# Kernel optimization log

Hardware: AMD Instinct MI355X
Metric: run time of the kernel (lower is better)

Reference implementation:

```python
import jax, jax.numpy as jnp
import numpy as np

DECAY = 0.99


def setup_inputs() -> dict:
    key = jax.random.key(0)
    k1, k2, k3 = jax.random.split(key, 3)
    B, L, D, N = 8, 2048, 512, 1024
    x = jax.random.normal(k1, (B, L, D), dtype=jnp.float32)
    codebook = jax.random.normal(k2, (N, D), dtype=jnp.float32)
    ema_weight = jax.random.normal(k3, (N, D), dtype=jnp.float32)
    counts = jnp.ones((N,), dtype=jnp.float32)
    return {"x": x, "codebook": codebook, "ema_weight": ema_weight, "counts": counts}


def reference(x, codebook, ema_weight, counts):
    # x: [B, L, D]; codebook/ema_weight: [N, D]; counts: [N]
    n_tokens = codebook.shape[0]
    # avoids materializing the [B,L,N,D] difference tensor of the naive form)
    x_sq = jnp.sum(x * x, axis=-1, keepdims=True)            # [B, L, 1]
    c_sq = jnp.sum(codebook * codebook, axis=-1)             # [N]
    xc = jnp.einsum('bld,nd->bln', x, codebook)              # [B, L, N]
    distances = jnp.sqrt(jnp.maximum(x_sq - 2.0 * xc + c_sq, 0.0))
    indices = jnp.argmin(distances, axis=-1)                 # [B, L]
    encodings = jax.nn.one_hot(indices, n_tokens, dtype=jnp.float32)  # [B, L, N]
    # train=True branch: EMA codebook update
    counts_new = DECAY * counts + (1.0 - DECAY) * jnp.sum(encodings, axis=(0, 1))
    dw = jnp.einsum('bln,bld->nd', encodings, x)             # [N, D]
    ema_new = DECAY * ema_weight + (1.0 - DECAY) * dw
    codebook_new = ema_new / counts_new[:, None]
    # quantization with straight-through estimator
    quantized = jnp.einsum('bln,nd->bld', encodings, codebook_new)  # [B, L, D]
    quantized = x + jax.lax.stop_gradient(quantized - x)
    # optax.l2_loss(x, quantized) = 0.5 * (x - quantized)^2
    codebook_loss = jnp.mean(0.5 * jnp.square(x - quantized))
    return quantized, codebook_loss, indices
```

## Files before the change

kernel.cpp:

```cpp
#include <hip/hip_runtime.h>
#include <hip/hip_bf16.h>

constexpr int Dd   = 512;
constexpr int Nn   = 1024;
constexpr int Ttok = 16384;
constexpr float DECAYc = 0.99f;
constexpr float MARGIN = 10.0f;
constexpr int CH = 16;

typedef short bf16x8 __attribute__((ext_vector_type(8)));
typedef float f32x4  __attribute__((ext_vector_type(4)));
typedef unsigned short us8v __attribute__((ext_vector_type(8)));

__device__ inline unsigned short f2bf(float f) {
  unsigned int b = __float_as_uint(f);
  return (unsigned short)((b + 0x7FFFu + ((b >> 16) & 1u)) >> 16);
}
__device__ inline float bf2f(unsigned short u) {
  return __uint_as_float(((unsigned int)u) << 16);
}

__global__ __launch_bounds__(64) void k_prep_cb(const float* __restrict__ cb,
                                                unsigned short* __restrict__ cbh,
                                                float* __restrict__ csq) {
  const int n = blockIdx.x, l = threadIdx.x;
  const float4* r = (const float4*)(cb + (size_t)n * Dd);
  float4 a = r[l], b = r[l + 64];
  float ss = a.x*a.x + a.y*a.y + a.z*a.z + a.w*a.w
           + b.x*b.x + b.y*b.y + b.z*b.z + b.w*b.w;
  ushort4 ua, ub;
  ua.x = f2bf(a.x); ua.y = f2bf(a.y); ua.z = f2bf(a.z); ua.w = f2bf(a.w);
  ub.x = f2bf(b.x); ub.y = f2bf(b.y); ub.z = f2bf(b.z); ub.w = f2bf(b.w);
  ((ushort4*)(cbh + (size_t)n * Dd))[l]      = ua;
  ((ushort4*)(cbh + (size_t)n * Dd))[l + 64] = ub;
#pragma unroll
  for (int o = 32; o; o >>= 1) ss += __shfl_down(ss, o);
  if (l == 0) csq[n] = ss;
}

__global__ __launch_bounds__(256) void k_gemm_scores(
    const unsigned short* __restrict__ cbh, const float* __restrict__ x,
    const float* __restrict__ csq, unsigned short* __restrict__ S) {
  __shared__ unsigned short As[128 * 64];
  __shared__ unsigned short Bs[128 * 64];
  const int tid = threadIdx.x;
  const int w = tid >> 6, l = tid & 63;
  const int b = blockIdx.x;
  const int s = (b & 7) * 128 + (b >> 3);
  const int cm = s & 7;
  const int tn = s >> 3;
  const int wr = w >> 1, wc = w & 1;

  const int srow = tid >> 3;
  const int xorw = (tid >> 3) & 7;
  const int scolA = ((tid & 7) ^ xorw) * 8;
  const int scolB = (tid & 7) * 8;
  const int wcolB = ((tid & 7) ^ xorw) * 8;

  f32x4 acc[4][4] = {};

  const unsigned short* gA0 = cbh + (size_t)(cm * 128) * Dd;
  const float*          gB0 = x   + (size_t)(tn * 128) * Dd;

  us8v bq[4];
#define LOADB(KC) do {                                                        \
    const int k0_ = (KC) * 64;                                                \
    _Pragma("unroll")                                                         \
    for (int p = 0; p < 4; ++p) {                                             \
      const float* gb = gB0 + (size_t)(p * 32 + srow) * Dd + k0_ + scolB;     \
      float4 v0 = *(const float4*)gb;                                         \
      float4 v1 = *(const float4*)(gb + 4);                                   \
      us8v o;                                                                 \
      o[0]=f2bf(v0.x); o[1]=f2bf(v0.y); o[2]=f2bf(v0.z); o[3]=f2bf(v0.w);     \
      o[4]=f2bf(v1.x); o[5]=f2bf(v1.y); o[6]=f2bf(v1.z); o[7]=f2bf(v1.w);     \
      bq[p] = o;                                                              \
    }                                                                         \
  } while (0)

  LOADB(0);

  for (int kc = 0; kc < Dd / 64; ++kc) {
    const int k0 = kc * 64;
    __syncthreads();
#pragma unroll
    for (int c = 0; c < 4; ++c) {
      const unsigned short* ga = gA0 + (size_t)(c * 32 + srow) * Dd + k0 + scolA;
      char* la = (char*)As + c * 4096 + w * 1024;
      __builtin_amdgcn_global_load_lds((const __attribute__((address_space(1))) void*)ga,
                                       (__attribute__((address_space(3))) void*)la, 16, 0, 0);
    }
#pragma unroll
    for (int p = 0; p < 4; ++p)
      *(us8v*)&Bs[(p * 32 + srow) * 64 + wcolB] = bq[p];
    __syncthreads();
    if (kc + 1 < Dd / 64) LOADB(kc + 1);
#pragma unroll
    for (int ks = 0; ks < 2; ++ks) {
      const int ra = l & 15;
      const int rx = l & 7;
      const int kbs = ((ks * 4 + (l >> 4)) ^ rx) * 8;
      bf16x8 af[4], bfr[4];
#pragma unroll
      for (int m = 0; m < 4; ++m)
        af[m] = *(const bf16x8*)&As[(wr * 64 + m * 16 + ra) * 64 + kbs];
#pragma unroll
      for (int n = 0; n < 4; ++n)
        bfr[n] = *(const bf16x8*)&Bs[(wc * 64 + n * 16 + ra) * 64 + kbs];
#pragma unroll
      for (int m = 0; m < 4; ++m)
#pragma unroll
        for (int n = 0; n < 4; ++n)
          acc[m][n] = __builtin_amdgcn_mfma_f32_16x16x32_bf16(af[m], bfr[n], acc[m][n], 0, 0, 0);
    }
  }
#undef LOADB

  const int code0 = cm * 128 + wr * 64 + (l >> 4) * 4;
  const int tok0  = tn * 128 + wc * 64 + (l & 15);
#pragma unroll
  for (int m = 0; m < 4; ++m) {
    const int cd = code0 + m * 16;
    float4 cs = *(const float4*)&csq[cd];
#pragma unroll
    for (int n = 0; n < 4; ++n) {
      const int tk = tok0 + n * 16;
      ushort4 o;
      o.x = f2bf(cs.x - 2.0f * acc[m][n][0]);
      o.y = f2bf(cs.y - 2.0f * acc[m][n][1]);
      o.z = f2bf(cs.z - 2.0f * acc[m][n][2]);
      o.w = f2bf(cs.w - 2.0f * acc[m][n][3]);
      *(ushort4*)(S + (size_t)tk * Nn + cd) = o;
    }
  }
}

__global__ __launch_bounds__(256) void k_scan(
    const unsigned short* __restrict__ S, const float* __restrict__ x,
    const float* __restrict__ cb, const float* __restrict__ csq,
    int* __restrict__ idxb, float* __restrict__ idxf, float* __restrict__ hist) {
  __shared__ int candn[4][32];
  __shared__ int ccnt[4];
  const int tid = threadIdx.x, wid = tid >> 6, l = tid & 63;
  const int t = blockIdx.x * 4 + wid;

  const unsigned short* row = S + (size_t)t * Nn;
  us8v c0 = *(const us8v*)(row + l * 8);
  us8v c1 = *(const us8v*)(row + 512 + l * 8);
  float f0[8], f1[8];
  float minv = 3.4e38f; int mini = 0;
#pragma unroll
  for (int j = 0; j < 8; ++j) {
    f0[j] = bf2f(c0[j]);
    if (f0[j] < minv) { minv = f0[j]; mini = l * 8 + j; }
  }
#pragma unroll
  for (int j = 0; j < 8; ++j) {
    f1[j] = bf2f(c1[j]);
    if (f1[j] < minv) { minv = f1[j]; mini = 512 + l * 8 + j; }
  }
#pragma unroll
  for (int o = 1; o < 64; o <<= 1) {
    float ov = __shfl_xor(minv, o); int oi = __shfl_xor(mini, o);
    if (ov < minv || (ov == minv && oi < mini)) { minv = ov; mini = oi; }
  }
  if (l == 0) ccnt[wid] = 0;
  const float thr = minv + MARGIN;
#pragma unroll
  for (int j = 0; j < 8; ++j)
    if (f0[j] <= thr) { int p = atomicAdd(&ccnt[wid], 1); if (p < 32) candn[wid][p] = l * 8 + j; }
#pragma unroll
  for (int j = 0; j < 8; ++j)
    if (f1[j] <= thr) { int p = atomicAdd(&ccnt[wid], 1); if (p < 32) candn[wid][p] = 512 + l * 8 + j; }
  int nc = ccnt[wid]; if (nc > 32) nc = 32;

  int besti;
  if (nc == 1) {
    besti = candn[wid][0];
  } else {
    float bestv = 3.4e38f; besti = 0x7fffffff;
    const float4* xr = (const float4*)(x + (size_t)t * Dd);
    float4 xa = xr[l * 2], xb = xr[l * 2 + 1];
    for (int c = 0; c < nc; ++c) {
      int n = candn[wid][c];
      const float4* cr = (const float4*)(cb + (size_t)n * Dd);
      float4 ca = cr[l * 2], cb4 = cr[l * 2 + 1];
      float p = xa.x*ca.x + xa.y*ca.y + xa.z*ca.z + xa.w*ca.w
              + xb.x*cb4.x + xb.y*cb4.y + xb.z*cb4.z + xb.w*cb4.w;
#pragma unroll
      for (int o = 32; o; o >>= 1) p += __shfl_xor(p, o);
      float sc = csq[n] - 2.0f * p;
      if (sc < bestv || (sc == bestv && n < besti)) { bestv = sc; besti = n; }
    }
  }
  if (l == 0) {
    idxb[t] = besti;
    idxf[t] = (float)besti;
    atomicAdd(&hist[besti], 1.0f);
  }
}

__global__ __launch_bounds__(256) void k_offsets(const float* __restrict__ hist,
                                                 int* __restrict__ offs,
                                                 int* __restrict__ cursor) {
  __shared__ int wsum[4];
  const int tid = threadIdx.x, l = tid & 63, wd = tid >> 6;
  const int base = tid * 4;
  int c0 = (int)hist[base], c1 = (int)hist[base + 1],
      c2 = (int)hist[base + 2], c3 = (int)hist[base + 3];
  int sum = c0 + c1 + c2 + c3;
  int sc = sum;
#pragma unroll
  for (int o = 1; o < 64; o <<= 1) { int v = __shfl_up(sc, o); if (l >= o) sc += v; }
  if (l == 63) wsum[wd] = sc;
  __syncthreads();
  int wbase = 0;
  for (int i = 0; i < wd; ++i) wbase += wsum[i];
  int e = wbase + sc - sum;
  offs[base] = e;     cursor[base] = e;
  offs[base+1] = e + c0; cursor[base+1] = e + c0;
  offs[base+2] = e + c0 + c1; cursor[base+2] = e + c0 + c1;
  offs[base+3] = e + c0 + c1 + c2; cursor[base+3] = e + c0 + c1 + c2;
}

__global__ __launch_bounds__(256) void k_scatter(const int* __restrict__ idxb,
                                                 int* __restrict__ cursor,
                                                 int* __restrict__ bucket,
                                                 int* __restrict__ bcode) {
  int t = blockIdx.x * 256 + threadIdx.x;
  if (t < Ttok) {
    int n = idxb[t];
    int p = atomicAdd(&cursor[n], 1);
    bucket[p] = t;
    bcode[p] = n;
  }
}

__global__ __launch_bounds__(512) void k_dw_part(
    const float* __restrict__ x, const int* __restrict__ bucket,
    const int* __restrict__ bcode, float* __restrict__ dw) {
  __shared__ int sh_t[CH], sh_n[CH];
  const int tid = threadIdx.x;
  const int p0 = blockIdx.x * CH;
  if (tid < CH) { sh_t[tid] = bucket[p0 + tid]; sh_n[tid] = bcode[p0 + tid]; }
  __syncthreads();
  float v[CH];
#pragma unroll
  for (int j = 0; j < CH; ++j)
    v[j] = x[(size_t)sh_t[j] * Dd + tid];
  float acc = v[0]; int cur = sh_n[0];
#pragma unroll
  for (int j = 1; j < CH; ++j) {
    int n = sh_n[j];
    if (n != cur) { atomicAdd(&dw[(size_t)cur * Dd + tid], acc); acc = 0.f; cur = n; }
    acc += v[j];
  }
  atomicAdd(&dw[(size_t)cur * Dd + tid], acc);
}

__global__ __launch_bounds__(256) void finalize_cb(
    const float* __restrict__ ema, const float* __restrict__ dw,
    const float* __restrict__ counts, const float* __restrict__ hist,
    float* __restrict__ cbnew) {
  int e4 = blockIdx.x * 256 + threadIdx.x;
  int n = e4 >> 7;
  float cnt = DECAYc * counts[n] + (1.0f - DECAYc) * hist[n];
  float inv = 1.0f / cnt;
  float4 e = ((const float4*)ema)[e4];
  float4 d = ((const float4*)dw)[e4];
  float4 o;
  o.x = (DECAYc * e.x + (1.0f - DECAYc) * d.x) * inv;
  o.y = (DECAYc * e.y + (1.0f - DECAYc) * d.y) * inv;
  o.z = (DECAYc * e.z + (1.0f - DECAYc) * d.z) * inv;
  o.w = (DECAYc * e.w + (1.0f - DECAYc) * d.w) * inv;
  ((float4*)cbnew)[e4] = o;
}

__global__ __launch_bounds__(256) void quant_loss(
    const float* __restrict__ x, const float* __restrict__ cbnew,
    const int* __restrict__ idx, float* __restrict__ out_q,
    float* __restrict__ loss) {
  const int e0 = blockIdx.x * 256 + threadIdx.x;
  const int gsz = 524288;
  int n[4]; float4 q[4], xv[4];
#pragma unroll
  for (int j = 0; j < 4; ++j) n[j] = idx[(e0 + j * gsz) >> 7];
#pragma unroll
  for (int j = 0; j < 4; ++j) {
    const int e = e0 + j * gsz;
    q[j]  = ((const float4*)(cbnew + (size_t)n[j] * Dd))[e & 127];
    xv[j] = ((const float4*)x)[e];
  }
  float part = 0.f;
#pragma unroll
  for (int j = 0; j < 4; ++j) {
    ((float4*)out_q)[e0 + j * gsz] = q[j];
    float dx = xv[j].x - q[j].x, dy = xv[j].y - q[j].y,
          dz = xv[j].z - q[j].z, dw_ = xv[j].w - q[j].w;
    part += dx*dx + dy*dy + dz*dz + dw_*dw_;
  }
  __shared__ float red[4];
#pragma unroll
  for (int o = 32; o; o >>= 1) part += __shfl_down(part, o);
  int wid = threadIdx.x >> 6, lane = threadIdx.x & 63;
  if (lane == 0) red[wid] = part;
  __syncthreads();
  if (threadIdx.x == 0) atomicAdd(loss, red[0] + red[1] + red[2] + red[3]);
}

__global__ void loss_final(const float* __restrict__ loss,
                           float* __restrict__ out_loss) {
  *out_loss = loss[0] * (0.5f / (float)((size_t)Ttok * Dd));
}

extern "C" void kernel_launch(void* const* d_in, const int* in_sizes, int n_in,
                              void* d_out, int out_size, void* d_ws, size_t ws_size,
                              hipStream_t stream) {
  const float* x      = (const float*)d_in[0];
  const float* cb     = (const float*)d_in[1];
  const float* ema    = (const float*)d_in[2];
  const float* counts = (const float*)d_in[3];

  float* out      = (float*)d_out;
  float* q_out    = out;
  float* loss_out = out + (size_t)Ttok * Dd;
  float* idxf_out = loss_out + 1;
  unsigned short* S = (unsigned short*)q_out;

  float* ws = (float*)d_ws;
  unsigned short* cbh = (unsigned short*)ws;
  float* dw      = ws + 262144;
  float* hist    = ws + 786432;
  float* loss    = ws + 787456;
  float* csq     = ws + 787460;
  int*   offs    = (int*)(ws + 788484);
  int*   cursor  = (int*)(ws + 789508);
  int*   bucket  = (int*)(ws + 790532);
  int*   bcode   = (int*)(ws + 806916);
  int*   idxb    = (int*)(ws + 823300);
  float* cbnew   = ws + 839684;

  hipMemsetAsync(dw, 0, (size_t)525316 * sizeof(float), stream);

  k_prep_cb<<<Nn, 64, 0, stream>>>(cb, cbh, csq);
  k_gemm_scores<<<(Nn / 128) * (Ttok / 128), 256, 0, stream>>>(cbh, x, csq, S);
  k_scan<<<Ttok / 4, 256, 0, stream>>>(S, x, cb, csq, idxb, idxf_out, hist);
  k_offsets<<<1, 256, 0, stream>>>(hist, offs, cursor);
  k_scatter<<<Ttok / 256, 256, 0, stream>>>(idxb, cursor, bucket, bcode);
  k_dw_part<<<Ttok / CH, 512, 0, stream>>>(x, bucket, bcode, dw);
  finalize_cb<<<(Nn * Dd / 4) / 256, 256, 0, stream>>>(ema, dw, counts, hist, cbnew);
  quant_loss<<<2048, 256, 0, stream>>>(x, cbnew, idxb, q_out, loss);
  loss_final<<<1, 1, 0, stream>>>(loss, loss_out);
}
```

Baseline: 126.5 us.

## Fuse top-2 argmin reduction into score GEMM epilogue and double-buffer A tiles

The GEMM epilogue no longer writes the full bf16 score matrix. For each 128-code slice it computes a per-token top-2 with a count of near-minimum candidates and writes one compact float4 per token. A new select kernel merges the 8 slices and rescores the few candidates exactly in fp32, falling back to a full 128-code rescan when a slice has many near-ties. This removes the large score-matrix write and read. It also double-buffers the codebook LDS tile so the next A load overlaps compute, at the cost of more shared memory and extra epilogue work.

Result: slower. 495.9 us (+291.9%).

```diff
diff --git a/kernel.cpp b/kernel.cpp
--- a/kernel.cpp
+++ b/kernel.cpp
@@ -15,9 +15,6 @@
 __device__ inline unsigned short f2bf(float f) {
   unsigned int b = __float_as_uint(f);
   return (unsigned short)((b + 0x7FFFu + ((b >> 16) & 1u)) >> 16);
-}
-__device__ inline float bf2f(unsigned short u) {
-  return __uint_as_float(((unsigned int)u) << 16);
 }
 
 __global__ __launch_bounds__(64) void k_prep_cb(const float* __restrict__ cb,
@@ -40,9 +37,10 @@
 
 __global__ __launch_bounds__(256) void k_gemm_scores(
     const unsigned short* __restrict__ cbh, const float* __restrict__ x,
-    const float* __restrict__ csq, unsigned short* __restrict__ S) {
-  __shared__ unsigned short As[128 * 64];
+    const float* __restrict__ csq, float4* __restrict__ part) {
+  __shared__ unsigned short As[2][128 * 64];
   __shared__ unsigned short Bs[128 * 64];
+  __shared__ float4 red4[2][128];
   const int tid = threadIdx.x;
   const int w = tid >> 6, l = tid & 63;
   const int b = blockIdx.x;
@@ -68,32 +66,39 @@
     _Pragma("unroll")                                                         \
     for (int p = 0; p < 4; ++p) {                                             \
       const float* gb = gB0 + (size_t)(p * 32 + srow) * Dd + k0_ + scolB;     \
-      float4 v0 = *(const float4*)gb;                                         \
-      float4 v1 = *(const float4*)(gb + 4);                                   \
+      float4 v0_ = *(const float4*)gb;                                        \
+      float4 v1_ = *(const float4*)(gb + 4);                                  \
       us8v o;                                                                 \
-      o[0]=f2bf(v0.x); o[1]=f2bf(v0.y); o[2]=f2bf(v0.z); o[3]=f2bf(v0.w);     \
-      o[4]=f2bf(v1.x); o[5]=f2bf(v1.y); o[6]=f2bf(v1.z); o[7]=f2bf(v1.w);     \
+      o[0]=f2bf(v0_.x); o[1]=f2bf(v0_.y); o[2]=f2bf(v0_.z); o[3]=f2bf(v0_.w); \
+      o[4]=f2bf(v1_.x); o[5]=f2bf(v1_.y); o[6]=f2bf(v1_.z); o[7]=f2bf(v1_.w); \
       bq[p] = o;                                                              \
     }                                                                         \
   } while (0)
-
+#define ISSUEA(KC, BUF) do {                                                  \
+    const int k0_ = (KC) * 64;                                                \
+    _Pragma("unroll")                                                         \
+    for (int c = 0; c < 4; ++c) {                                             \
+      const unsigned short* ga = gA0 + (size_t)(c * 32 + srow) * Dd + k0_ + scolA; \
+      char* la = (char*)&As[BUF][0] + c * 4096 + w * 1024;                    \
+      __builtin_amdgcn_global_load_lds((const __attribute__((address_space(1))) void*)ga, \
+                                       (__attribute__((address_space(3))) void*)la, 16, 0, 0); \
+    }                                                                         \
+  } while (0)
+
+  ISSUEA(0, 0);
   LOADB(0);
 
   for (int kc = 0; kc < Dd / 64; ++kc) {
-    const int k0 = kc * 64;
     __syncthreads();
-#pragma unroll
-    for (int c = 0; c < 4; ++c) {
-      const unsigned short* ga = gA0 + (size_t)(c * 32 + srow) * Dd + k0 + scolA;
-      char* la = (char*)As + c * 4096 + w * 1024;
-      __builtin_amdgcn_global_load_lds((const __attribute__((address_space(1))) void*)ga,
-                                       (__attribute__((address_space(3))) void*)la, 16, 0, 0);
-    }
 #pragma unroll
     for (int p = 0; p < 4; ++p)
       *(us8v*)&Bs[(p * 32 + srow) * 64 + wcolB] = bq[p];
     __syncthreads();
-    if (kc + 1 < Dd / 64) LOADB(kc + 1);
+    if (kc + 1 < Dd / 64) {
+      ISSUEA(kc + 1, (kc + 1) & 1);
+      LOADB(kc + 1);
+    }
+    const unsigned short* Ab = &As[kc & 1][0];
 #pragma unroll
     for (int ks = 0; ks < 2; ++ks) {
       const int ra = l & 15;
@@ -102,7 +107,7 @@
       bf16x8 af[4], bfr[4];
 #pragma unroll
       for (int m = 0; m < 4; ++m)
-        af[m] = *(const bf16x8*)&As[(wr * 64 + m * 16 + ra) * 64 + kbs];
+        af[m] = *(const bf16x8*)&Ab[(wr * 64 + m * 16 + ra) * 64 + kbs];
 #pragma unroll
       for (int n = 0; n < 4; ++n)
         bfr[n] = *(const bf16x8*)&Bs[(wc * 64 + n * 16 + ra) * 64 + kbs];
@@ -114,82 +119,116 @@
     }
   }
 #undef LOADB
-
-  const int code0 = cm * 128 + wr * 64 + (l >> 4) * 4;
-  const int tok0  = tn * 128 + wc * 64 + (l & 15);
-#pragma unroll
-  for (int m = 0; m < 4; ++m) {
-    const int cd = code0 + m * 16;
-    float4 cs = *(const float4*)&csq[cd];
-#pragma unroll
-    for (int n = 0; n < 4; ++n) {
-      const int tk = tok0 + n * 16;
-      ushort4 o;
-      o.x = f2bf(cs.x - 2.0f * acc[m][n][0]);
-      o.y = f2bf(cs.y - 2.0f * acc[m][n][1]);
-      o.z = f2bf(cs.z - 2.0f * acc[m][n][2]);
-      o.w = f2bf(cs.w - 2.0f * acc[m][n][3]);
-      *(ushort4*)(S + (size_t)tk * Nn + cd) = o;
-    }
-  }
-}
-
-__global__ __launch_bounds__(256) void k_scan(
-    const unsigned short* __restrict__ S, const float* __restrict__ x,
+#undef ISSUEA
+
+  const int base4 = wr * 64 + (l >> 4) * 4;
+  float4 cs[4];
+#pragma unroll
+  for (int m = 0; m < 4; ++m)
+    cs[m] = *(const float4*)&csq[cm * 128 + base4 + m * 16];
+
+#pragma unroll
+  for (int n = 0; n < 4; ++n) {
+    float v0 = 3.4e38f, v1 = 3.4e38f;
+    int i0 = 0x7fffffff, i1 = 0x7fffffff;
+#pragma unroll
+    for (int m = 0; m < 4; ++m) {
+#pragma unroll
+      for (int r = 0; r < 4; ++r) {
+        float sv = fmaf(-2.0f, acc[m][n][r], ((const float*)&cs[m])[r]);
+        int idx = cm * 128 + base4 + m * 16 + r;
+        if (sv < v0)      { v1 = v0; i1 = i0; v0 = sv; i0 = idx; }
+        else if (sv < v1) { v1 = sv; i1 = idx; }
+      }
+    }
+#pragma unroll
+    for (int o = 16; o <= 32; o <<= 1) {
+      float b0 = __shfl_xor(v0, o), b1 = __shfl_xor(v1, o);
+      int  bi0 = __shfl_xor(i0, o), bi1 = __shfl_xor(i1, o);
+      bool bf = (b0 < v0) || (b0 == v0 && bi0 < i0);
+      float lo = bf ? v0 : b0; int loi = bf ? i0 : bi0;
+      float w1 = bf ? b1 : v1; int w1i = bf ? bi1 : i1;
+      if (bf) { v0 = b0; i0 = bi0; }
+      bool sf = (lo < w1) || (lo == w1 && loi < w1i);
+      v1 = sf ? lo : w1; i1 = sf ? loi : w1i;
+    }
+    int c16 = 0; const float thr = v0 + MARGIN;
+#pragma unroll
+    for (int m = 0; m < 4; ++m)
+#pragma unroll
+      for (int r = 0; r < 4; ++r)
+        c16 += (fmaf(-2.0f, acc[m][n][r], ((const float*)&cs[m])[r]) <= thr) ? 1 : 0;
+    c16 += __shfl_xor(c16, 16); c16 += __shfl_xor(c16, 32);
+    if ((l >> 4) == 0)
+      red4[wr][wc * 64 + n * 16 + l] = make_float4(
+          v0, v1, __uint_as_float((unsigned)i0 | ((unsigned)i1 << 16)),
+          __uint_as_float((unsigned)c16));
+  }
+  __syncthreads();
+  if (tid < 128) {
+    float4 a = red4[0][tid], e = red4[1][tid];
+    unsigned au = __float_as_uint(a.z), eu = __float_as_uint(e.z);
+    int ai0 = au & 0xffff, ai1 = au >> 16;
+    int ei0 = eu & 0xffff, ei1 = eu >> 16;
+    bool bf = (e.x < a.x) || (e.x == a.x && ei0 < ai0);
+    float v0 = bf ? e.x : a.x; int i0 = bf ? ei0 : ai0;
+    float lo = bf ? a.x : e.x; int loi = bf ? ai0 : ei0;
+    float w1 = bf ? e.y : a.y; int w1i = bf ? ei1 : ai1;
+    bool sf = (lo < w1) || (lo == w1 && loi < w1i);
+    float v1 = sf ? lo : w1; int i1 = sf ? loi : w1i;
+    unsigned cnt = __float_as_uint(a.w) + __float_as_uint(e.w);
+    part[(size_t)cm * Ttok + tn * 128 + tid] = make_float4(
+        v0, v1, __uint_as_float((unsigned)i0 | ((unsigned)i1 << 16)),
+        __uint_as_float(cnt));
+  }
+}
+
+__device__ inline void rescore(int n, const float4& xa, const float4& xb,
+                               const float* __restrict__ cb,
+                               const float* __restrict__ csq, int l,
+                               float& bestv, int& besti) {
+  const float4* cr = (const float4*)(cb + (size_t)n * Dd);
+  float4 ca = cr[l * 2], cc = cr[l * 2 + 1];
+  float p = xa.x*ca.x + xa.y*ca.y + xa.z*ca.z + xa.w*ca.w
+          + xb.x*cc.x + xb.y*cc.y + xb.z*cc.z + xb.w*cc.w;
+#pragma unroll
+  for (int o = 32; o; o >>= 1) p += __shfl_xor(p, o);
+  float sc = csq[n] - 2.0f * p;
+  if (sc < bestv || (sc == bestv && n < besti)) { bestv = sc; besti = n; }
+}
+
+__global__ __launch_bounds__(256) void k_select(
+    const float4* __restrict__ part, const float* __restrict__ x,
     const float* __restrict__ cb, const float* __restrict__ csq,
     int* __restrict__ idxb, float* __restrict__ idxf, float* __restrict__ hist) {
-  __shared__ int candn[4][32];
-  __shared__ int ccnt[4];
   const int tid = threadIdx.x, wid = tid >> 6, l = tid & 63;
   const int t = blockIdx.x * 4 + wid;
-
-  const unsigned short* row = S + (size_t)t * Nn;
-  us8v c0 = *(const us8v*)(row + l * 8);
-  us8v c1 = *(const us8v*)(row + 512 + l * 8);
-  float f0[8], f1[8];
-  float minv = 3.4e38f; int mini = 0;
-#pragma unroll
-  for (int j = 0; j < 8; ++j) {
-    f0[j] = bf2f(c0[j]);
-    if (f0[j] < minv) { minv = f0[j]; mini = l * 8 + j; }
-  }
-#pragma unroll
-  for (int j = 0; j < 8; ++j) {
-    f1[j] = bf2f(c1[j]);
-    if (f1[j] < minv) { minv = f1[j]; mini = 512 + l * 8 + j; }
-  }
-#pragma unroll
-  for (int o = 1; o < 64; o <<= 1) {
-    float ov = __shfl_xor(minv, o); int oi = __shfl_xor(mini, o);
-    if (ov < minv || (ov == minv && oi < mini)) { minv = ov; mini = oi; }
-  }
-  if (l == 0) ccnt[wid] = 0;
-  const float thr = minv + MARGIN;
-#pragma unroll
-  for (int j = 0; j < 8; ++j)
-    if (f0[j] <= thr) { int p = atomicAdd(&ccnt[wid], 1); if (p < 32) candn[wid][p] = l * 8 + j; }
-#pragma unroll
-  for (int j = 0; j < 8; ++j)
-    if (f1[j] <= thr) { int p = atomicAdd(&ccnt[wid], 1); if (p < 32) candn[wid][p] = 512 + l * 8 + j; }
-  int nc = ccnt[wid]; if (nc > 32) nc = 32;
-
-  int besti;
-  if (nc == 1) {
-    besti = candn[wid][0];
-  } else {
-    float bestv = 3.4e38f; besti = 0x7fffffff;
-    const float4* xr = (const float4*)(x + (size_t)t * Dd);
-    float4 xa = xr[l * 2], xb = xr[l * 2 + 1];
-    for (int c = 0; c < nc; ++c) {
-      int n = candn[wid][c];
-      const float4* cr = (const float4*)(cb + (size_t)n * Dd);
-      float4 ca = cr[l * 2], cb4 = cr[l * 2 + 1];
-      float p = xa.x*ca.x + xa.y*ca.y + xa.z*ca.z + xa.w*ca.w
-              + xb.x*cb4.x + xb.y*cb4.y + xb.z*cb4.z + xb.w*cb4.w;
-#pragma unroll
-      for (int o = 32; o; o >>= 1) p += __shfl_xor(p, o);
-      float sc = csq[n] - 2.0f * p;
-      if (sc < bestv || (sc == bestv && n < besti)) { bestv = sc; besti = n; }
+  float v0 = 3.4e38f, v1 = 3.4e38f; unsigned ii = 0, cnt = 0;
+  if (l < 8) {
+    float4 e = part[(size_t)l * Ttok + t];
+    v0 = e.x; v1 = e.y; ii = __float_as_uint(e.z); cnt = __float_as_uint(e.w);
+  }
+  float m = v0;
+#pragma unroll
+  for (int o = 1; o < 8; o <<= 1) m = fminf(m, __shfl_xor(m, o));
+  m = __shfl(m, 0);
+  const float thr = m + MARGIN;
+  const float4* xr = (const float4*)(x + (size_t)t * Dd);
+  float4 xa = xr[l * 2], xb = xr[l * 2 + 1];
+  float bestv = 3.4e38f; int besti = 0x7fffffff;
+  for (int b = 0; b < 8; ++b) {
+    float vb0 = __shfl(v0, b);
+    if (vb0 > thr) continue;
+    unsigned cntb = __shfl(cnt, b);
+    unsigned iib  = __shfl(ii, b);
+    float vb1     = __shfl(v1, b);
+    if (cntb <= 2) {
+      rescore((int)(iib & 0xffff), xa, xb, cb, csq, l, bestv, besti);
+      if (vb1 <= thr)
+        rescore((int)(iib >> 16), xa, xb, cb, csq, l, bestv, besti);
+    } else {
+      for (int c = 0; c < 128; ++c)
+        rescore(b * 128 + c, xa, xb, cb, csq, l, bestv, besti);
     }
   }
   if (l == 0) {
@@ -324,7 +363,7 @@
   float* q_out    = out;
   float* loss_out = out + (size_t)Ttok * Dd;
   float* idxf_out = loss_out + 1;
-  unsigned short* S = (unsigned short*)q_out;
+  float4* part = (float4*)q_out;
 
   float* ws = (float*)d_ws;
   unsigned short* cbh = (unsigned short*)ws;
@@ -342,8 +381,8 @@
   hipMemsetAsync(dw, 0, (size_t)525316 * sizeof(float), stream);
 
   k_prep_cb<<<Nn, 64, 0, stream>>>(cb, cbh, csq);
-  k_gemm_scores<<<(Nn / 128) * (Ttok / 128), 256, 0, stream>>>(cbh, x, csq, S);
-  k_scan<<<Ttok / 4, 256, 0, stream>>>(S, x, cb, csq, idxb, idxf_out, hist);
+  k_gemm_scores<<<(Nn / 128) * (Ttok / 128), 256, 0, stream>>>(cbh, x, csq, part);
+  k_select<<<Ttok / 4, 256, 0, stream>>>(part, x, cb, csq, idxb, idxf_out, hist);
   k_offsets<<<1, 256, 0, stream>>>(hist, offs, cursor);
   k_scatter<<<Ttok / 256, 256, 0, stream>>>(idxb, cursor, bucket, bcode);
   k_dw_part<<<Ttok / CH, 512, 0, stream>>>(x, bucket, bcode, dw);
```
